# Kernel optimization log

Measured on AMD Instinct MI355X. Metric: run time of the kernel, lower is better.

The kernel has to match this reference:

```python
import jax, jax.numpy as jnp
import numpy as np

LAMBDA_COORD = 5.0
LAMBDA_NOOBJ = 0.5
GRID = 7
IMG = 448.0
CELL = IMG / GRID  # 64.0
EPS = 1e-06


def setup_inputs() -> dict:
    key = jax.random.key(0)
    k1, k2, k3 = jax.random.split(key, 3)
    B = 16384
    # predictions in [0.05, 1) so sqrt(w), sqrt(h) are well-behaved (as in training)
    input_ = jax.random.uniform(k1, (B, 30, GRID, GRID), dtype=jnp.float32, minval=0.05, maxval=1.0)
    target = jax.random.uniform(k2, (B, GRID, GRID, 30), dtype=jnp.float32, minval=0.05, maxval=1.0)
    # objectness target must be exactly 1.0 for 'has object' cells (code tests == 1)
    has_obj = (jax.random.uniform(k3, (B, GRID, GRID)) > 0.7).astype(jnp.float32)
    target = target.at[:, :, :, 4].set(has_obj)
    return {"input_": input_, "target": target}


def _corners(rows30, col, row):
    # rows30: [N,30] cell-relative preds; col/row: [N] grid indices
    # returns x1,y1,x2,y2 each [N,2] (two boxes per cell), clipped to image
    cx = rows30[:, jnp.array([0, 5])] * CELL + (col * CELL)[:, None]
    cy = rows30[:, jnp.array([1, 6])] * CELL + (row * CELL)[:, None]
    w = rows30[:, jnp.array([2, 7])] * IMG
    h = rows30[:, jnp.array([3, 8])] * IMG
    x1 = jnp.clip(cx - w / 2, 0.0, IMG)
    y1 = jnp.clip(cy - h / 2, 0.0, IMG)
    x2 = jnp.clip(cx + w / 2, 0.0, IMG)
    y2 = jnp.clip(cy + h / 2, 0.0, IMG)
    return x1, y1, x2, y2


def _yolo_loss(input_, target):
    B = input_.shape[0]
    # [B,30,7,7] -> [B,7,7,30] -> [N,30]
    x = jnp.transpose(input_, (0, 2, 3, 1)).reshape(-1, 30)
    t = target.reshape(-1, 30)
    N = x.shape[0]

    # grid offsets: flat index = b*49 + row*7 + col
    cell_idx = jnp.arange(GRID * GRID)
    col = jnp.tile((cell_idx % GRID).astype(x.dtype), B)  # [N]
    row = jnp.tile((cell_idx // GRID).astype(x.dtype), B)  # [N]

    ix1, iy1, ix2, iy2 = _corners(x, col, row)
    tx1, ty1, tx2, ty2 = _corners(t, col, row)

    # IoU of each predicted box vs same-slot target box, [N,2]
    iw = jnp.maximum(jnp.minimum(ix2, tx2) - jnp.maximum(ix1, tx1), EPS)
    ih = jnp.maximum(jnp.minimum(iy2, ty2) - jnp.maximum(iy1, ty1), EPS)
    inter = iw * ih
    area_sum = (ix2 - ix1) * (iy2 - iy1) + (tx2 - tx1) * (ty2 - ty1)
    iou2 = inter / (area_sum - inter)  # [N,2]

    m = iou2[:, 0] < iou2[:, 1]                       # box 1 selected where True
    iou = jnp.where(m, iou2[:, 1], iou2[:, 0])        # [N]

    has_obj = (t[:, 4] == 1.0).astype(x.dtype)        # [N]
    no_obj = 1.0 - has_obj

    sel = jnp.where(m[:, None], x[:, 5:10], x[:, :5])  # [N,5] selected box

    coordinate_error = jnp.sum(has_obj * ((sel[:, 0] - t[:, 0]) ** 2 + (sel[:, 1] - t[:, 1]) ** 2))
    size_error = jnp.sum(has_obj * ((jnp.sqrt(sel[:, 2]) - jnp.sqrt(t[:, 2])) ** 2
                                    + (jnp.sqrt(sel[:, 3]) - jnp.sqrt(t[:, 3])) ** 2))
    confidence_error = jnp.sum(has_obj * (sel[:, 4] - iou) ** 2)
    classification_error = jnp.sum(has_obj[:, None] * (x[:, 10:] - t[:, 10:]) ** 2)
    noobj_confidence_error = jnp.sum(no_obj * (x[:, 4] ** 2 + x[:, 9] ** 2))

    loss = (LAMBDA_COORD * coordinate_error + LAMBDA_COORD * size_error
            + confidence_error + LAMBDA_NOOBJ * noobj_confidence_error
            + classification_error)
    return loss / B


def reference(input_, target):
    return _yolo_loss(input_, target)
```

## Files before the change

### kernel.cpp

```cpp
#include <hip/hip_runtime.h>


#define CELLF   64.0f
#define IMGF    448.0f
#define EPSF    1e-6f
#define LAMBDA_COORD 5.0f
#define LAMBDA_NOOBJ 0.5f

#define TPB 256

__global__ __launch_bounds__(TPB) void yolo_main(
    const float* __restrict__ input,
    const float* __restrict__ target,
    float* __restrict__ partial,
    int ncells)
{
    const int tid = threadIdx.x;
    const int n   = blockIdx.x * TPB + tid;

    float lv = 0.0f;
    if (n < ncells) {
        const int b    = n / 49;
        const int cell = n - b * 49;
        const int row  = cell / 7;
        const int col  = cell - row * 7;

        const float* xin = input + (size_t)b * 1470 + cell;
        float x[30];
        #pragma unroll
        for (int c = 0; c < 30; ++c) x[c] = xin[c * 49];

        const float2* tp = reinterpret_cast<const float2*>(target + (size_t)n * 30);
        float t[30];
        #pragma unroll
        for (int j = 0; j < 15; ++j) {
            float2 v = tp[j];
            t[2 * j]     = v.x;
            t[2 * j + 1] = v.y;
        }

        __builtin_amdgcn_sched_barrier(0);

        const float colf = (float)col * CELLF;
        const float rowf = (float)row * CELLF;

        float iou[2];
        #pragma unroll
        for (int k = 0; k < 2; ++k) {
            const int o = 5 * k;
            float pcx = x[o + 0] * CELLF + colf;
            float pcy = x[o + 1] * CELLF + rowf;
            float pw  = x[o + 2] * IMGF;
            float ph  = x[o + 3] * IMGF;
            float px1 = fminf(fmaxf(pcx - 0.5f * pw, 0.0f), IMGF);
            float py1 = fminf(fmaxf(pcy - 0.5f * ph, 0.0f), IMGF);
            float px2 = fminf(fmaxf(pcx + 0.5f * pw, 0.0f), IMGF);
            float py2 = fminf(fmaxf(pcy + 0.5f * ph, 0.0f), IMGF);

            float tcx = t[o + 0] * CELLF + colf;
            float tcy = t[o + 1] * CELLF + rowf;
            float tw  = t[o + 2] * IMGF;
            float th  = t[o + 3] * IMGF;
            float tx1 = fminf(fmaxf(tcx - 0.5f * tw, 0.0f), IMGF);
            float ty1 = fminf(fmaxf(tcy - 0.5f * th, 0.0f), IMGF);
            float tx2 = fminf(fmaxf(tcx + 0.5f * tw, 0.0f), IMGF);
            float ty2 = fminf(fmaxf(tcy + 0.5f * th, 0.0f), IMGF);

            float iw = fmaxf(fminf(px2, tx2) - fmaxf(px1, tx1), EPSF);
            float ih = fmaxf(fminf(py2, ty2) - fmaxf(py1, ty1), EPSF);
            float inter = iw * ih;
            float area  = (px2 - px1) * (py2 - py1) + (tx2 - tx1) * (ty2 - ty1);
            iou[k] = inter / (area - inter);
        }

        const bool  m      = iou[0] < iou[1];
        const float iouSel = m ? iou[1] : iou[0];
        const float has_obj = (t[4] == 1.0f) ? 1.0f : 0.0f;
        const float no_obj  = 1.0f - has_obj;

        const float s0 = m ? x[5] : x[0];
        const float s1 = m ? x[6] : x[1];
        const float s2 = m ? x[7] : x[2];
        const float s3 = m ? x[8] : x[3];
        const float s4 = m ? x[9] : x[4];

        float d0 = s0 - t[0], d1 = s1 - t[1];
        float coord_e = d0 * d0 + d1 * d1;

        float e2 = sqrtf(s2) - sqrtf(t[2]);
        float e3 = sqrtf(s3) - sqrtf(t[3]);
        float size_e = e2 * e2 + e3 * e3;

        float dc = s4 - iouSel;
        float conf_e = dc * dc;

        float cls_e = 0.0f;
        #pragma unroll
        for (int c = 10; c < 30; ++c) {
            float d = x[c] - t[c];
            cls_e += d * d;
        }

        float noobj_e = x[4] * x[4] + x[9] * x[9];

        lv = has_obj * (LAMBDA_COORD * coord_e + LAMBDA_COORD * size_e + conf_e + cls_e)
           + LAMBDA_NOOBJ * no_obj * noobj_e;
    }

    #pragma unroll
    for (int off = 32; off > 0; off >>= 1)
        lv += __shfl_down(lv, off, 64);

    __shared__ float s_part[TPB / 64];
    if ((tid & 63) == 0) s_part[tid >> 6] = lv;
    __syncthreads();

    if (tid == 0) {
        float tot = 0.0f;
        #pragma unroll
        for (int w = 0; w < TPB / 64; ++w) tot += s_part[w];
        partial[blockIdx.x] = tot;
    }
}

__global__ __launch_bounds__(256) void yolo_reduce(
    const float* __restrict__ partial, int nparts,
    float* __restrict__ out, float inv_b)
{
    const int tid = threadIdx.x;
    float v = 0.0f;
    for (int i = tid; i < nparts; i += 256) v += partial[i];

    #pragma unroll
    for (int off = 32; off > 0; off >>= 1)
        v += __shfl_down(v, off, 64);

    __shared__ float s_part[4];
    if ((tid & 63) == 0) s_part[tid >> 6] = v;
    __syncthreads();

    if (tid == 0)
        out[0] = (s_part[0] + s_part[1] + s_part[2] + s_part[3]) * inv_b;
}

extern "C" void kernel_launch(void* const* d_in, const int* in_sizes, int n_in,
                              void* d_out, int out_size, void* d_ws, size_t ws_size,
                              hipStream_t stream) {
    const float* input  = (const float*)d_in[0];
    const float* target = (const float*)d_in[1];
    float* out = (float*)d_out;
    float* partial = (float*)d_ws;

    const int B = in_sizes[0] / (30 * 49);
    const int ncells = B * 49;
    const int nblocks = (ncells + TPB - 1) / TPB;

    yolo_main<<<nblocks, TPB, 0, stream>>>(input, target, partial, ncells);
    yolo_reduce<<<1, 256, 0, stream>>>(partial, nblocks, out, 1.0f / (float)B);
}
```

Before: 206.2 us.

## Stage input and target tiles in LDS via direct global-to-LDS loads

Each block now handles four whole images (196 cells). Their contiguous input and target data is copied into shared memory using global_load_lds with 16-byte lanes, plus a 4-byte tail, so the global reads are fully coalesced instead of strided per cell. Each thread then reads its channels from LDS. The cost is that 60 of the 256 threads sit idle, each block uses about 47 KB of LDS, which limits occupancy, and B must be divisible by 4.

Result: no change. 207.1 us (+0.5%).

```diff
diff --git a/kernel.cpp b/kernel.cpp
--- a/kernel.cpp
+++ b/kernel.cpp
@@ -7,39 +7,69 @@
 #define LAMBDA_COORD 5.0f
 #define LAMBDA_NOOBJ 0.5f
 
-#define TPB 256
+#define TPB        256
+#define BPB        4
+#define CELLS_PB   (BPB * 49)
+#define FLOATS_PB  (BPB * 1470)
+#define WBYTES     (FLOATS_PB * 4)
+#define NCHUNK     (WBYTES >> 10)
+#define TAILOFF    (NCHUNK << 10)
+#define NTAILDW    ((WBYTES - TAILOFF) >> 2)
 
 __global__ __launch_bounds__(TPB) void yolo_main(
     const float* __restrict__ input,
     const float* __restrict__ target,
-    float* __restrict__ partial,
-    int ncells)
+    float* __restrict__ partial)
 {
-    const int tid = threadIdx.x;
-    const int n   = blockIdx.x * TPB + tid;
+    __shared__ float s_in[FLOATS_PB];
+    __shared__ float s_tg[FLOATS_PB];
+    __shared__ float s_part[TPB / 64];
+
+    const int tid  = threadIdx.x;
+    const int wid  = tid >> 6;
+    const int lane = tid & 63;
+
+    const size_t base_f = (size_t)blockIdx.x * FLOATS_PB;
+    const char* gin = (const char*)(input  + base_f);
+    const char* gtg = (const char*)(target + base_f);
+
+    for (int c = wid; c < NCHUNK; c += TPB / 64) {
+        const int off = c << 10;
+        __builtin_amdgcn_global_load_lds((const float*)(gin + off + lane * 16),
+                                         (float*)((char*)s_in + off), 16, 0, 0);
+        __builtin_amdgcn_global_load_lds((const float*)(gtg + off + lane * 16),
+                                         (float*)((char*)s_tg + off), 16, 0, 0);
+    }
+    if (wid == (NCHUNK & 3)) {
+        #pragma unroll
+        for (int d = 0; d < NTAILDW; d += 64) {
+            const int idx = d + lane;
+            if (idx < NTAILDW) {
+                __builtin_amdgcn_global_load_lds((const float*)(gin + TAILOFF + idx * 4),
+                                                 (float*)((char*)s_in + TAILOFF + d * 4), 4, 0, 0);
+                __builtin_amdgcn_global_load_lds((const float*)(gtg + TAILOFF + idx * 4),
+                                                 (float*)((char*)s_tg + TAILOFF + d * 4), 4, 0, 0);
+            }
+        }
+    }
+    __syncthreads();
 
     float lv = 0.0f;
-    if (n < ncells) {
-        const int b    = n / 49;
-        const int cell = n - b * 49;
+    if (tid < CELLS_PB) {
+        const int db   = tid / 49;
+        const int cell = tid - db * 49;
         const int row  = cell / 7;
         const int col  = cell - row * 7;
 
-        const float* xin = input + (size_t)b * 1470 + cell;
+        const float* xin = s_in + db * 1470 + cell;
         float x[30];
         #pragma unroll
         for (int c = 0; c < 30; ++c) x[c] = xin[c * 49];
 
-        const float2* tp = reinterpret_cast<const float2*>(target + (size_t)n * 30);
-        float t[30];
+        const float* t = s_tg + tid * 30;
+        float tt[30];
         #pragma unroll
-        for (int j = 0; j < 15; ++j) {
-            float2 v = tp[j];
-            t[2 * j]     = v.x;
-            t[2 * j + 1] = v.y;
-        }
-
-        __builtin_amdgcn_sched_barrier(0);
+        for (int j = 0; j < 30; ++j) tt[j] = t[j];
 
         const float colf = (float)col * CELLF;
         const float rowf = (float)row * CELLF;
@@ -57,10 +87,10 @@
             float px2 = fminf(fmaxf(pcx + 0.5f * pw, 0.0f), IMGF);
             float py2 = fminf(fmaxf(pcy + 0.5f * ph, 0.0f), IMGF);
 
-            float tcx = t[o + 0] * CELLF + colf;
-            float tcy = t[o + 1] * CELLF + rowf;
-            float tw  = t[o + 2] * IMGF;
-            float th  = t[o + 3] * IMGF;
+            float tcx = tt[o + 0] * CELLF + colf;
+            float tcy = tt[o + 1] * CELLF + rowf;
+            float tw  = tt[o + 2] * IMGF;
+            float th  = tt[o + 3] * IMGF;
             float tx1 = fminf(fmaxf(tcx - 0.5f * tw, 0.0f), IMGF);
             float ty1 = fminf(fmaxf(tcy - 0.5f * th, 0.0f), IMGF);
             float tx2 = fminf(fmaxf(tcx + 0.5f * tw, 0.0f), IMGF);
@@ -75,7 +105,7 @@
 
         const bool  m      = iou[0] < iou[1];
         const float iouSel = m ? iou[1] : iou[0];
-        const float has_obj = (t[4] == 1.0f) ? 1.0f : 0.0f;
+        const float has_obj = (tt[4] == 1.0f) ? 1.0f : 0.0f;
         const float no_obj  = 1.0f - has_obj;
 
         const float s0 = m ? x[5] : x[0];
@@ -84,11 +114,11 @@
         const float s3 = m ? x[8] : x[3];
         const float s4 = m ? x[9] : x[4];
 
-        float d0 = s0 - t[0], d1 = s1 - t[1];
+        float d0 = s0 - tt[0], d1 = s1 - tt[1];
         float coord_e = d0 * d0 + d1 * d1;
 
-        float e2 = sqrtf(s2) - sqrtf(t[2]);
-        float e3 = sqrtf(s3) - sqrtf(t[3]);
+        float e2 = sqrtf(s2) - sqrtf(tt[2]);
+        float e3 = sqrtf(s3) - sqrtf(tt[3]);
         float size_e = e2 * e2 + e3 * e3;
 
         float dc = s4 - iouSel;
@@ -97,7 +127,7 @@
         float cls_e = 0.0f;
         #pragma unroll
         for (int c = 10; c < 30; ++c) {
-            float d = x[c] - t[c];
+            float d = x[c] - tt[c];
             cls_e += d * d;
         }
 
@@ -111,7 +141,6 @@
     for (int off = 32; off > 0; off >>= 1)
         lv += __shfl_down(lv, off, 64);
 
-    __shared__ float s_part[TPB / 64];
     if ((tid & 63) == 0) s_part[tid >> 6] = lv;
     __syncthreads();
 
@@ -152,9 +181,8 @@
     float* partial = (float*)d_ws;
 
     const int B = in_sizes[0] / (30 * 49);
-    const int ncells = B * 49;
-    const int nblocks = (ncells + TPB - 1) / TPB;
+    const int nblocks = B / BPB;
 
-    yolo_main<<<nblocks, TPB, 0, stream>>>(input, target, partial, ncells);
+    yolo_main<<<nblocks, TPB, 0, stream>>>(input, target, partial);
     yolo_reduce<<<1, 256, 0, stream>>>(partial, nblocks, out, 1.0f / (float)B);
 }
```
